# Kernel tuning notes

Measured on AMD Instinct MI355X. Metric: run time of the kernel, lower is better.

The kernel has to match this reference:

```python
import jax, jax.numpy as jnp
import numpy as np

N, E = 50000, 800000
IN, HID, HEADS, OUT, ED = 128, 64, 2, 64, 32
NEG_SLOPE = 0.2


def setup_inputs() -> dict:
    key = jax.random.key(0)
    ks = jax.random.split(key, 16)
    g = lambda i, shape: (jax.random.normal(ks[i], shape, jnp.float32) * 0.05)
    return {
        "x": g(0, (N, IN)),
        "edge_index": jax.random.randint(ks[1], (2, E), 0, N, jnp.int32),
        "edge_attr": g(2, (E, ED)),
        # layer 1 (heads=HEADS, out=HID)
        "Wl1": g(3, (IN, HEADS * HID)), "bl1": jnp.zeros((HEADS * HID,), jnp.float32),
        "Wr1": g(4, (IN, HEADS * HID)), "br1": jnp.zeros((HEADS * HID,), jnp.float32),
        "We1": g(5, (ED, HEADS * HID)),
        "att1": g(6, (HEADS, HID)),
        "bias1": jnp.zeros((HEADS * HID,), jnp.float32),
        # layer 2 (heads=1, out=OUT)
        "Wl2": g(7, (HEADS * HID, OUT)), "bl2": jnp.zeros((OUT,), jnp.float32),
        "Wr2": g(8, (HEADS * HID, OUT)), "br2": jnp.zeros((OUT,), jnp.float32),
        "We2": g(9, (ED, OUT)),
        "att2": g(10, (1, OUT)),
        "bias2": jnp.zeros((OUT,), jnp.float32),
    }


def _add_self_loops(src, dst, edge_attr, n):
    # PyG add_self_loops(fill_value='mean'): self-loop attr = mean of incoming edge attrs
    ones = jnp.ones((src.shape[0],), edge_attr.dtype)
    deg = jax.ops.segment_sum(ones, dst, num_segments=n)
    loop_attr = jax.ops.segment_sum(edge_attr, dst, num_segments=n) / jnp.maximum(deg, 1.0)[:, None]
    idx = jnp.arange(n, dtype=src.dtype)
    return (jnp.concatenate([src, idx]), jnp.concatenate([dst, idx]),
            jnp.concatenate([edge_attr, loop_attr], axis=0))


def _gatv2_layer(x, src, dst, edge_attr, Wl, bl, Wr, br, We, att, bias, heads, out_c):
    n = x.shape[0]
    xl = (x @ Wl + bl).reshape(n, heads, out_c)   # applied to source nodes j
    xr = (x @ Wr + br).reshape(n, heads, out_c)   # applied to target nodes i
    e = (edge_attr @ We).reshape(-1, heads, out_c)
    m = jax.nn.leaky_relu(xl[src] + xr[dst] + e, NEG_SLOPE)   # [E', H, C]
    logits = jnp.einsum('ehc,hc->eh', m, att)                  # [E', H]
    # segment softmax over incoming edges of each target node
    lmax = jax.ops.segment_max(logits, dst, num_segments=n)
    lmax = jnp.where(jnp.isfinite(lmax), lmax, 0.0)
    ex = jnp.exp(logits - lmax[dst])
    denom = jax.ops.segment_sum(ex, dst, num_segments=n)
    alpha = ex / (denom[dst] + 1e-16)                          # [E', H]
    out = jax.ops.segment_sum(xl[src] * alpha[:, :, None], dst, num_segments=n)
    return out.reshape(n, heads * out_c) + bias                # concat=True


def reference(x, edge_index, edge_attr,
              Wl1, bl1, Wr1, br1, We1, att1, bias1,
              Wl2, bl2, Wr2, br2, We2, att2, bias2):
    n = x.shape[0]
    src, dst, ea = _add_self_loops(edge_index[0], edge_index[1], edge_attr, n)
    h = _gatv2_layer(x, src, dst, ea, Wl1, bl1, Wr1, br1, We1, att1, bias1, HEADS, HID)
    h = jax.nn.elu(h)
    out = _gatv2_layer(h, src, dst, ea, Wl2, bl2, Wr2, br2, We2, att2, bias2, 1, OUT)
    return out
```

## Files before the change

kernel.cpp:

```cpp
#include <hip/hip_runtime.h>
#include <cmath>

#define NN 50000
#define EE 800000
#define H1C 128
#define OUTC 64
#define EDIM 32
#define NBLK 196

__device__ __forceinline__ float bcast(float v, int d) {
    return __int_as_float(__builtin_amdgcn_readlane(__float_as_int(v), d));
}


__global__ void k_hist(const int* __restrict__ ei, int* deg) {
    int e = blockIdx.x * 256 + threadIdx.x;
    if (e < EE) atomicAdd(&deg[ei[EE + e]], 1);
}

__global__ void k_scan_block(const int* __restrict__ deg, int* offs, int* bsum) {
    __shared__ int s[256];
    int t = threadIdx.x;
    int gid = blockIdx.x * 256 + t;
    int v = (gid < NN) ? deg[gid] : 0;
    s[t] = v;
    __syncthreads();
    for (int off = 1; off < 256; off <<= 1) {
        int add = (t >= off) ? s[t - off] : 0;
        __syncthreads();
        s[t] += add;
        __syncthreads();
    }
    if (gid < NN) offs[gid] = s[t] - v;
    if (t == 255) bsum[blockIdx.x] = s[255];
}

__global__ void k_scan_top(const int* __restrict__ bsum, int* bexcl) {
    __shared__ int s[256];
    int t = threadIdx.x;
    int v = (t < NBLK) ? bsum[t] : 0;
    s[t] = v;
    __syncthreads();
    for (int off = 1; off < 256; off <<= 1) {
        int add = (t >= off) ? s[t - off] : 0;
        __syncthreads();
        s[t] += add;
        __syncthreads();
    }
    bexcl[t] = s[t] - v;
}

__global__ void k_scan_add(int* offs, const int* __restrict__ bexcl) {
    int gid = blockIdx.x * 256 + threadIdx.x;
    if (gid < NN) offs[gid] += bexcl[blockIdx.x];
    if (gid == 0) offs[NN] = EE;
}

__global__ void k_scatter(const int* __restrict__ ei, const int* __restrict__ offs,
                          int* deg, int2* esort) {
    int e = blockIdx.x * 256 + threadIdx.x;
    if (e >= EE) return;
    int dst = ei[EE + e];
    int idx = atomicSub(&deg[dst], 1) - 1;
    esort[offs[dst] + idx] = make_int2(ei[e], e);
}


template <int MO, bool IL>
__global__ void k_lin_pair(const float* __restrict__ x,
                           const float* __restrict__ Wa, const float* __restrict__ ba,
                           const float* __restrict__ Wb, const float* __restrict__ bb,
                           float* __restrict__ oa, float* __restrict__ ob) {
    __shared__ float xsT[128][36];
    int n0 = blockIdx.x * 32;
    int nthr = 2 * MO;
    for (int idx = threadIdx.x; idx < 32 * 128; idx += nthr) {
        int n = idx >> 7, k = idx & 127;
        xsT[k][n] = (n0 + n < NN) ? x[(size_t)(n0 + n) * 128 + k] : 0.f;
    }
    __syncthreads();
    int t = threadIdx.x;
    const float* W  = (t < MO) ? Wa : Wb;
    const float* bp = (t < MO) ? ba : bb;
    float* op       = (t < MO) ? oa : ob;
    int m = (t < MO) ? t : t - MO;
    float bv = bp[m];
    float acc[32];
#pragma unroll
    for (int n = 0; n < 32; ++n) acc[n] = bv;
#pragma unroll 2
    for (int k = 0; k < 128; ++k) {
        float w = W[k * MO + m];
        const float4* row = reinterpret_cast<const float4*>(&xsT[k][0]);
#pragma unroll
        for (int c = 0; c < 8; ++c) {
            float4 v = row[c];
            acc[4 * c + 0] = fmaf(v.x, w, acc[4 * c + 0]);
            acc[4 * c + 1] = fmaf(v.y, w, acc[4 * c + 1]);
            acc[4 * c + 2] = fmaf(v.z, w, acc[4 * c + 2]);
            acc[4 * c + 3] = fmaf(v.w, w, acc[4 * c + 3]);
        }
    }
    int mo = IL ? (((m & 63) << 1) + (m >> 6)) : m;
#pragma unroll
    for (int n = 0; n < 32; ++n)
        if (n0 + n < NN) op[(size_t)(n0 + n) * MO + mo] = acc[n];
}


__device__ __forceinline__ void edge_upd1(float2 xlv, float av,
                                          float2 xrv, float a0, float a1,
                                          const float (&wr0)[32], const float (&wr1)[32],
                                          float& mr0, float& mr1, float& s0, float& s1,
                                          float& acc0, float& acc1) {
    float t0 = 0.f, t1 = 0.f, u0 = 0.f, u1 = 0.f;
#pragma unroll
    for (int d = 0; d < 16; ++d) {
        float a = bcast(av, d);
        t0 = fmaf(a, wr0[d], t0);
        t1 = fmaf(a, wr1[d], t1);
    }
#pragma unroll
    for (int d = 16; d < 32; ++d) {
        float a = bcast(av, d);
        u0 = fmaf(a, wr0[d], u0);
        u1 = fmaf(a, wr1[d], u1);
    }
    float m0 = (xlv.x + xrv.x) + (t0 + u0);
    float m1 = (xlv.y + xrv.y) + (t1 + u1);
    m0 = m0 > 0.f ? m0 : 0.2f * m0;
    m1 = m1 > 0.f ? m1 : 0.2f * m1;
    float p0 = m0 * a0, p1 = m1 * a1;
#pragma unroll
    for (int off = 32; off; off >>= 1) { p0 += __shfl_xor(p0, off); p1 += __shfl_xor(p1, off); }
    float nm = fmaxf(mr0, p0);
    float sc = __expf(mr0 - nm), e = __expf(p0 - nm);
    s0 = s0 * sc + e; acc0 = fmaf(acc0, sc, e * xlv.x); mr0 = nm;
    nm = fmaxf(mr1, p1);
    sc = __expf(mr1 - nm); e = __expf(p1 - nm);
    s1 = s1 * sc + e; acc1 = fmaf(acc1, sc, e * xlv.y); mr1 = nm;
}

__global__ void __launch_bounds__(256) k_l1(
    const int2* __restrict__ esort, const int* __restrict__ offs,
    const float* __restrict__ ea, const float* __restrict__ We,
    const float* __restrict__ att, const float* __restrict__ xl,
    const float* __restrict__ xr, const float* __restrict__ bias,
    float* __restrict__ hb) {
    int lane = threadIdx.x & 63;
    float wr0[32], wr1[32];
#pragma unroll
    for (int d = 0; d < 32; ++d) {
        wr0[d] = We[d * H1C + lane];
        wr1[d] = We[d * H1C + 64 + lane];
    }
    int dst = (blockIdx.x << 2) + (threadIdx.x >> 6);
    if (dst >= NN) return;
    int beg = offs[dst], end = offs[dst + 1];
    int n = end - beg;
    float a0 = att[lane], a1 = att[64 + lane];
    size_t db = (size_t)dst * H1C;
    float2 xrv = reinterpret_cast<const float2*>(xr + db)[lane];
    float mr0 = -INFINITY, mr1 = -INFINITY;
    float s0 = 0.f, s1 = 0.f, acc0 = 0.f, acc1 = 0.f, easum = 0.f;

    float2 xlv = make_float2(0.f, 0.f);
    float av = 0.f;
    if (n > 0) {
        int2 ed = esort[beg];
        xlv = reinterpret_cast<const float2*>(xl + (size_t)ed.x * H1C)[lane];
        av = ea[(size_t)ed.y * EDIM + (lane & 31)];
    }
    for (int j = beg; j < end; ++j) {
        float2 cxl = xlv; float cav = av;
        if (j + 1 < end) {
            int2 ed = esort[j + 1];
            xlv = reinterpret_cast<const float2*>(xl + (size_t)ed.x * H1C)[lane];
            av = ea[(size_t)ed.y * EDIM + (lane & 31)];
        }
        easum += cav;
        edge_upd1(cxl, cav, xrv, a0, a1, wr0, wr1, mr0, mr1, s0, s1, acc0, acc1);
    }

    float lav = easum * ((n > 0) ? (1.f / (float)n) : 1.f);
    float2 sxl = reinterpret_cast<const float2*>(xl + db)[lane];
    edge_upd1(sxl, lav, xrv, a0, a1, wr0, wr1, mr0, mr1, s0, s1, acc0, acc1);

    float h0 = acc0 / (s0 + 1e-16f) + bias[lane];
    float h1 = acc1 / (s1 + 1e-16f) + bias[64 + lane];
    hb[db + lane]      = h0 > 0.f ? h0 : expm1f(h0);
    hb[db + 64 + lane] = h1 > 0.f ? h1 : expm1f(h1);
}


__device__ __forceinline__ void edge_upd2(float xlv, float av, float xrv, float a,
                                          const float (&wr)[32],
                                          float& mr, float& s, float& acc) {
    float t = 0.f, u = 0.f;
#pragma unroll
    for (int d = 0; d < 16; ++d)
        t = fmaf(bcast(av, d), wr[d], t);
#pragma unroll
    for (int d = 16; d < 32; ++d)
        u = fmaf(bcast(av, d), wr[d], u);
    float m = (xlv + xrv) + (t + u);
    m = m > 0.f ? m : 0.2f * m;
    float p = m * a;
#pragma unroll
    for (int off = 32; off; off >>= 1) p += __shfl_xor(p, off);
    float nm = fmaxf(mr, p);
    float sc = __expf(mr - nm), e = __expf(p - nm);
    s = s * sc + e; acc = fmaf(acc, sc, e * xlv); mr = nm;
}

__global__ void __launch_bounds__(256) k_l2(
    const int2* __restrict__ esort, const int* __restrict__ offs,
    const float* __restrict__ ea, const float* __restrict__ We,
    const float* __restrict__ att, const float* __restrict__ xl,
    const float* __restrict__ xr, const float* __restrict__ bias,
    float* __restrict__ out) {
    int lane = threadIdx.x & 63;
    float wr[32];
#pragma unroll
    for (int d = 0; d < 32; ++d) wr[d] = We[d * OUTC + lane];
    int dst = (blockIdx.x << 2) + (threadIdx.x >> 6);
    if (dst >= NN) return;
    int beg = offs[dst], end = offs[dst + 1];
    int n = end - beg;
    float a = att[lane];
    size_t db = (size_t)dst * OUTC;
    float xrv = xr[db + lane];
    float mr = -INFINITY, s = 0.f, acc = 0.f, easum = 0.f;

    float xlv = 0.f, av = 0.f;
    if (n > 0) {
        int2 ed = esort[beg];
        xlv = xl[(size_t)ed.x * OUTC + lane];
        av = ea[(size_t)ed.y * EDIM + (lane & 31)];
    }
    for (int j = beg; j < end; ++j) {
        float cxl = xlv, cav = av;
        if (j + 1 < end) {
            int2 ed = esort[j + 1];
            xlv = xl[(size_t)ed.x * OUTC + lane];
            av = ea[(size_t)ed.y * EDIM + (lane & 31)];
        }
        easum += cav;
        edge_upd2(cxl, cav, xrv, a, wr, mr, s, acc);
    }
    float lav = easum * ((n > 0) ? (1.f / (float)n) : 1.f);
    float sxl = xl[db + lane];
    edge_upd2(sxl, lav, xrv, a, wr, mr, s, acc);

    out[db + lane] = acc / (s + 1e-16f) + bias[lane];
}


extern "C" void kernel_launch(void* const* d_in, const int* in_sizes, int n_in,
                              void* d_out, int out_size, void* d_ws, size_t ws_size,
                              hipStream_t stream) {
    const float* x    = (const float*)d_in[0];
    const int*   ei   = (const int*)d_in[1];
    const float* ea   = (const float*)d_in[2];
    const float* Wl1  = (const float*)d_in[3];
    const float* bl1  = (const float*)d_in[4];
    const float* Wr1  = (const float*)d_in[5];
    const float* br1  = (const float*)d_in[6];
    const float* We1  = (const float*)d_in[7];
    const float* att1 = (const float*)d_in[8];
    const float* bias1= (const float*)d_in[9];
    const float* Wl2  = (const float*)d_in[10];
    const float* bl2  = (const float*)d_in[11];
    const float* Wr2  = (const float*)d_in[12];
    const float* br2  = (const float*)d_in[13];
    const float* We2  = (const float*)d_in[14];
    const float* att2 = (const float*)d_in[15];
    const float* bias2= (const float*)d_in[16];
    float* out = (float*)d_out;

    char* w = (char*)d_ws;
    int2* esort = (int2*)w;                 w += (size_t)EE * 8;
    int*  offs  = (int*)w;                  w += (size_t)(NN + 4) * 4;
    int*  bsum  = (int*)w;                  w += 256 * 4;
    int*  bexcl = (int*)w;                  w += 256 * 4;
    int*  deg   = (int*)w;                  w += (size_t)NN * 4;
    float* xl1  = (float*)w;                w += (size_t)NN * H1C * 4;
    float* xr1  = (float*)w;                w += (size_t)NN * H1C * 4;
    float* hb   = (float*)w;                w += (size_t)NN * H1C * 4;
    float* xl2  = (float*)w;                w += (size_t)NN * OUTC * 4;
    float* xr2  = (float*)w;                w += (size_t)NN * OUTC * 4;

    hipMemsetAsync(deg, 0, (size_t)NN * 4, stream);

    k_hist<<<(EE + 255) / 256, 256, 0, stream>>>(ei, deg);
    k_scan_block<<<NBLK, 256, 0, stream>>>(deg, offs, bsum);
    k_scan_top<<<1, 256, 0, stream>>>(bsum, bexcl);
    k_scan_add<<<NBLK, 256, 0, stream>>>(offs, bexcl);
    k_scatter<<<(EE + 255) / 256, 256, 0, stream>>>(ei, offs, deg, esort);

    k_lin_pair<128, true><<<(NN + 31) / 32, 256, 0, stream>>>(x, Wl1, bl1, Wr1, br1, xl1, xr1);
    k_l1<<<(NN + 3) / 4, 256, 0, stream>>>(esort, offs, ea, We1, att1, xl1, xr1, bias1, hb);

    k_lin_pair<64, false><<<(NN + 31) / 32, 128, 0, stream>>>(hb, Wl2, bl2, Wr2, br2, xl2, xr2);
    k_l2<<<(NN + 3) / 4, 256, 0, stream>>>(esort, offs, ea, We2, att2, xl2, xr2, bias2, out);
}
```

Measured before the change: 857.0 us.

## Use DPP wave reductions and two-deep prefetch in edge-aggregation kernels

Replaces the shuffle-based 64-lane reduction of attention logits with a DPP row/broadcast reduction sequence that ends in a readlane. The per-edge loops in both GATv2 layers now keep two edges in flight, splitting the edge-attribute projection from the softmax update so loads for edge j+2/j+3 are issued while the current edge is processed. Launch bounds add a minimum-occupancy hint of 4. The deeper prefetch raises register pressure, and the occupancy hint may force spills given the 64 weight registers per lane.

```diff
diff --git a/kernel.cpp b/kernel.cpp
--- a/kernel.cpp
+++ b/kernel.cpp
@@ -10,6 +10,21 @@
 
 __device__ __forceinline__ float bcast(float v, int d) {
     return __int_as_float(__builtin_amdgcn_readlane(__float_as_int(v), d));
+}
+
+template <int CTRL, int RM>
+__device__ __forceinline__ float dpp_add(float x) {
+    int y = __builtin_amdgcn_update_dpp(0, __float_as_int(x), CTRL, RM, 0xf, false);
+    return x + __int_as_float(y);
+}
+__device__ __forceinline__ float wsum64(float x) {
+    x = dpp_add<0x111, 0xf>(x);
+    x = dpp_add<0x112, 0xf>(x);
+    x = dpp_add<0x114, 0xf>(x);
+    x = dpp_add<0x118, 0xf>(x);
+    x = dpp_add<0x142, 0xa>(x);
+    x = dpp_add<0x143, 0xc>(x);
+    return __int_as_float(__builtin_amdgcn_readlane(__float_as_int(x), 63));
 }
 
 
@@ -108,11 +123,8 @@
 }
 
 
-__device__ __forceinline__ void edge_upd1(float2 xlv, float av,
-                                          float2 xrv, float a0, float a1,
-                                          const float (&wr0)[32], const float (&wr1)[32],
-                                          float& mr0, float& mr1, float& s0, float& s1,
-                                          float& acc0, float& acc1) {
+__device__ __forceinline__ void dot1(float av, const float (&wr0)[32], const float (&wr1)[32],
+                                     float& q0, float& q1) {
     float t0 = 0.f, t1 = 0.f, u0 = 0.f, u1 = 0.f;
 #pragma unroll
     for (int d = 0; d < 16; ++d) {
@@ -126,13 +138,19 @@
         u0 = fmaf(a, wr0[d], u0);
         u1 = fmaf(a, wr1[d], u1);
     }
-    float m0 = (xlv.x + xrv.x) + (t0 + u0);
-    float m1 = (xlv.y + xrv.y) + (t1 + u1);
+    q0 = t0 + u0; q1 = t1 + u1;
+}
+
+__device__ __forceinline__ void fin1(float2 xlv, float q0, float q1, float2 xrv,
+                                     float a0, float a1,
+                                     float& mr0, float& mr1, float& s0, float& s1,
+                                     float& acc0, float& acc1) {
+    float m0 = (xlv.x + xrv.x) + q0;
+    float m1 = (xlv.y + xrv.y) + q1;
     m0 = m0 > 0.f ? m0 : 0.2f * m0;
     m1 = m1 > 0.f ? m1 : 0.2f * m1;
-    float p0 = m0 * a0, p1 = m1 * a1;
-#pragma unroll
-    for (int off = 32; off; off >>= 1) { p0 += __shfl_xor(p0, off); p1 += __shfl_xor(p1, off); }
+    float p0 = wsum64(m0 * a0);
+    float p1 = wsum64(m1 * a1);
     float nm = fmaxf(mr0, p0);
     float sc = __expf(mr0 - nm), e = __expf(p0 - nm);
     s0 = s0 * sc + e; acc0 = fmaf(acc0, sc, e * xlv.x); mr0 = nm;
@@ -141,7 +159,7 @@
     s1 = s1 * sc + e; acc1 = fmaf(acc1, sc, e * xlv.y); mr1 = nm;
 }
 
-__global__ void __launch_bounds__(256) k_l1(
+__global__ void __launch_bounds__(256, 4) k_l1(
     const int2* __restrict__ esort, const int* __restrict__ offs,
     const float* __restrict__ ea, const float* __restrict__ We,
     const float* __restrict__ att, const float* __restrict__ xl,
@@ -164,27 +182,52 @@
     float mr0 = -INFINITY, mr1 = -INFINITY;
     float s0 = 0.f, s1 = 0.f, acc0 = 0.f, acc1 = 0.f, easum = 0.f;
 
-    float2 xlv = make_float2(0.f, 0.f);
-    float av = 0.f;
+    float2 xlA = make_float2(0.f, 0.f), xlB = make_float2(0.f, 0.f);
+    float avA = 0.f, avB = 0.f;
     if (n > 0) {
         int2 ed = esort[beg];
-        xlv = reinterpret_cast<const float2*>(xl + (size_t)ed.x * H1C)[lane];
-        av = ea[(size_t)ed.y * EDIM + (lane & 31)];
-    }
-    for (int j = beg; j < end; ++j) {
-        float2 cxl = xlv; float cav = av;
-        if (j + 1 < end) {
-            int2 ed = esort[j + 1];
-            xlv = reinterpret_cast<const float2*>(xl + (size_t)ed.x * H1C)[lane];
-            av = ea[(size_t)ed.y * EDIM + (lane & 31)];
-        }
-        easum += cav;
-        edge_upd1(cxl, cav, xrv, a0, a1, wr0, wr1, mr0, mr1, s0, s1, acc0, acc1);
+        xlA = reinterpret_cast<const float2*>(xl + (size_t)ed.x * H1C)[lane];
+        avA = ea[(size_t)ed.y * EDIM + (lane & 31)];
+    }
+    if (n > 1) {
+        int2 ed = esort[beg + 1];
+        xlB = reinterpret_cast<const float2*>(xl + (size_t)ed.x * H1C)[lane];
+        avB = ea[(size_t)ed.y * EDIM + (lane & 31)];
+    }
+    int j = beg;
+    for (; j + 2 <= end; j += 2) {
+        float q0, q1;
+        easum += avA;
+        dot1(avA, wr0, wr1, q0, q1);
+        float2 c = xlA;
+        if (j + 2 < end) {
+            int2 ed = esort[j + 2];
+            xlA = reinterpret_cast<const float2*>(xl + (size_t)ed.x * H1C)[lane];
+            avA = ea[(size_t)ed.y * EDIM + (lane & 31)];
+        }
+        fin1(c, q0, q1, xrv, a0, a1, mr0, mr1, s0, s1, acc0, acc1);
+        easum += avB;
+        dot1(avB, wr0, wr1, q0, q1);
+        float2 d2 = xlB;
+        if (j + 3 < end) {
+            int2 ed = esort[j + 3];
+            xlB = reinterpret_cast<const float2*>(xl + (size_t)ed.x * H1C)[lane];
+            avB = ea[(size_t)ed.y * EDIM + (lane & 31)];
+        }
+        fin1(d2, q0, q1, xrv, a0, a1, mr0, mr1, s0, s1, acc0, acc1);
+    }
+    if (j < end) {
+        float q0, q1;
+        easum += avA;
+        dot1(avA, wr0, wr1, q0, q1);
+        fin1(xlA, q0, q1, xrv, a0, a1, mr0, mr1, s0, s1, acc0, acc1);
     }
 
     float lav = easum * ((n > 0) ? (1.f / (float)n) : 1.f);
+    float q0, q1;
+    dot1(lav, wr0, wr1, q0, q1);
     float2 sxl = reinterpret_cast<const float2*>(xl + db)[lane];
-    edge_upd1(sxl, lav, xrv, a0, a1, wr0, wr1, mr0, mr1, s0, s1, acc0, acc1);
+    fin1(sxl, q0, q1, xrv, a0, a1, mr0, mr1, s0, s1, acc0, acc1);
 
     float h0 = acc0 / (s0 + 1e-16f) + bias[lane];
     float h1 = acc1 / (s1 + 1e-16f) + bias[64 + lane];
@@ -193,27 +236,26 @@
 }
 
 
-__device__ __forceinline__ void edge_upd2(float xlv, float av, float xrv, float a,
-                                          const float (&wr)[32],
-                                          float& mr, float& s, float& acc) {
+__device__ __forceinline__ float dot2(float av, const float (&wr)[32]) {
     float t = 0.f, u = 0.f;
 #pragma unroll
-    for (int d = 0; d < 16; ++d)
-        t = fmaf(bcast(av, d), wr[d], t);
-#pragma unroll
-    for (int d = 16; d < 32; ++d)
-        u = fmaf(bcast(av, d), wr[d], u);
-    float m = (xlv + xrv) + (t + u);
+    for (int d = 0; d < 16; ++d) t = fmaf(bcast(av, d), wr[d], t);
+#pragma unroll
+    for (int d = 16; d < 32; ++d) u = fmaf(bcast(av, d), wr[d], u);
+    return t + u;
+}
+
+__device__ __forceinline__ void fin2(float xlv, float q, float xrv, float a,
+                                     float& mr, float& s, float& acc) {
+    float m = (xlv + xrv) + q;
     m = m > 0.f ? m : 0.2f * m;
-    float p = m * a;
-#pragma unroll
-    for (int off = 32; off; off >>= 1) p += __shfl_xor(p, off);
+    float p = wsum64(m * a);
     float nm = fmaxf(mr, p);
     float sc = __expf(mr - nm), e = __expf(p - nm);
     s = s * sc + e; acc = fmaf(acc, sc, e * xlv); mr = nm;
 }
 
-__global__ void __launch_bounds__(256) k_l2(
+__global__ void __launch_bounds__(256, 4) k_l2(
     const int2* __restrict__ esort, const int* __restrict__ offs,
     const float* __restrict__ ea, const float* __restrict__ We,
     const float* __restrict__ att, const float* __restrict__ xl,
@@ -232,25 +274,48 @@
     float xrv = xr[db + lane];
     float mr = -INFINITY, s = 0.f, acc = 0.f, easum = 0.f;
 
-    float xlv = 0.f, av = 0.f;
+    float xlA = 0.f, xlB = 0.f, avA = 0.f, avB = 0.f;
     if (n > 0) {
         int2 ed = esort[beg];
-        xlv = xl[(size_t)ed.x * OUTC + lane];
-        av = ea[(size_t)ed.y * EDIM + (lane & 31)];
-    }
-    for (int j = beg; j < end; ++j) {
-        float cxl = xlv, cav = av;
-        if (j + 1 < end) {
-            int2 ed = esort[j + 1];
-            xlv = xl[(size_t)ed.x * OUTC + lane];
-            av = ea[(size_t)ed.y * EDIM + (lane & 31)];
-        }
-        easum += cav;
-        edge_upd2(cxl, cav, xrv, a, wr, mr, s, acc);
-    }
+        xlA = xl[(size_t)ed.x * OUTC + lane];
+        avA = ea[(size_t)ed.y * EDIM + (lane & 31)];
+    }
+    if (n > 1) {
+        int2 ed = esort[beg + 1];
+        xlB = xl[(size_t)ed.x * OUTC + lane];
+        avB = ea[(size_t)ed.y * EDIM + (lane & 31)];
+    }
+    int j = beg;
+    for (; j + 2 <= end; j += 2) {
+        easum += avA;
+        float q = dot2(avA, wr);
+        float c = xlA;
+        if (j + 2 < end) {
+            int2 ed = esort[j + 2];
+            xlA = xl[(size_t)ed.x * OUTC + lane];
+            avA = ea[(size_t)ed.y * EDIM + (lane & 31)];
+        }
+        fin2(c, q, xrv, a, mr, s, acc);
+        easum += avB;
+        q = dot2(avB, wr);
+        float d2 = xlB;
+        if (j + 3 < end) {
+            int2 ed = esort[j + 3];
+            xlB = xl[(size_t)ed.x * OUTC + lane];
+            avB = ea[(size_t)ed.y * EDIM + (lane & 31)];
+        }
+        fin2(d2, q, xrv, a, mr, s, acc);
+    }
+    if (j < end) {
+        easum += avA;
+        float q = dot2(avA, wr);
+        fin2(xlA, q, xrv, a, mr, s, acc);
+    }
+
     float lav = easum * ((n > 0) ? (1.f / (float)n) : 1.f);
+    float q = dot2(lav, wr);
     float sxl = xl[db + lane];
-    edge_upd2(sxl, lav, xrv, a, wr, mr, s, acc);
+    fin2(sxl, q, xrv, a, mr, s, acc);
 
     out[db + lane] = acc / (s + 1e-16f) + bias[lane];
 }
@@ -290,7 +355,7 @@
     float* xl2  = (float*)w;                w += (size_t)NN * OUTC * 4;
     float* xr2  = (float*)w;                w += (size_t)NN * OUTC * 4;
 
-    hipMemsetAsync(deg, 0, (size_t)NN * 4, stream);
+    (void)hipMemsetAsync(deg, 0, (size_t)NN * 4, stream);
 
     k_hist<<<(EE + 255) / 256, 256, 0, stream>>>(ei, deg);
     k_scan_block<<<NBLK, 256, 0, stream>>>(deg, offs, bsum);
```

Result: faster. 809.7 us (-5.5%).

## Split layer-1 heads across wavefronts, DPP reductions, 4-deep edge prefetch

Applied to the files above, without the earlier changes.

Layer 1 now runs one wavefront per (destination, head) instead of one per destination handling both heads. This halves per-thread registers (one 32-float weight array) and raises occupancy via launch bounds. The projection writes xl/xr in a head-major planar layout so each head's gathers are contiguous 64-float rows. Edge processing in both layers uses a shared 4-deep software-pipelined gather loop, and the per-edge logit reduction switches from shuffle-xor to DPP row ops plus readlane. The trade-off is that edge indices and edge attributes are now gathered twice in layer 1, once per head.

```diff
diff --git a/kernel.cpp b/kernel.cpp
--- a/kernel.cpp
+++ b/kernel.cpp
@@ -10,6 +10,21 @@
 
 __device__ __forceinline__ float bcast(float v, int d) {
     return __int_as_float(__builtin_amdgcn_readlane(__float_as_int(v), d));
+}
+
+template <int CTRL, int RM>
+__device__ __forceinline__ float dpp_add(float x) {
+    int y = __builtin_amdgcn_update_dpp(0, __float_as_int(x), CTRL, RM, 0xf, false);
+    return x + __int_as_float(y);
+}
+__device__ __forceinline__ float wsum64(float x) {
+    x = dpp_add<0x111, 0xf>(x);
+    x = dpp_add<0x112, 0xf>(x);
+    x = dpp_add<0x114, 0xf>(x);
+    x = dpp_add<0x118, 0xf>(x);
+    x = dpp_add<0x142, 0xa>(x);
+    x = dpp_add<0x143, 0xc>(x);
+    return __int_as_float(__builtin_amdgcn_readlane(__float_as_int(x), 63));
 }
 
 
@@ -66,7 +81,7 @@
 }
 
 
-template <int MO, bool IL>
+template <int MO, int MODE>
 __global__ void k_lin_pair(const float* __restrict__ x,
                            const float* __restrict__ Wa, const float* __restrict__ ba,
                            const float* __restrict__ Wb, const float* __restrict__ bb,
@@ -101,119 +116,105 @@
             acc[4 * c + 3] = fmaf(v.w, w, acc[4 * c + 3]);
         }
     }
-    int mo = IL ? (((m & 63) << 1) + (m >> 6)) : m;
-#pragma unroll
-    for (int n = 0; n < 32; ++n)
-        if (n0 + n < NN) op[(size_t)(n0 + n) * MO + mo] = acc[n];
-}
-
-
-__device__ __forceinline__ void edge_upd1(float2 xlv, float av,
-                                          float2 xrv, float a0, float a1,
-                                          const float (&wr0)[32], const float (&wr1)[32],
-                                          float& mr0, float& mr1, float& s0, float& s1,
-                                          float& acc0, float& acc1) {
-    float t0 = 0.f, t1 = 0.f, u0 = 0.f, u1 = 0.f;
-#pragma unroll
-    for (int d = 0; d < 16; ++d) {
-        float a = bcast(av, d);
-        t0 = fmaf(a, wr0[d], t0);
-        t1 = fmaf(a, wr1[d], t1);
-    }
-#pragma unroll
-    for (int d = 16; d < 32; ++d) {
-        float a = bcast(av, d);
-        u0 = fmaf(a, wr0[d], u0);
-        u1 = fmaf(a, wr1[d], u1);
-    }
-    float m0 = (xlv.x + xrv.x) + (t0 + u0);
-    float m1 = (xlv.y + xrv.y) + (t1 + u1);
-    m0 = m0 > 0.f ? m0 : 0.2f * m0;
-    m1 = m1 > 0.f ? m1 : 0.2f * m1;
-    float p0 = m0 * a0, p1 = m1 * a1;
-#pragma unroll
-    for (int off = 32; off; off >>= 1) { p0 += __shfl_xor(p0, off); p1 += __shfl_xor(p1, off); }
-    float nm = fmaxf(mr0, p0);
-    float sc = __expf(mr0 - nm), e = __expf(p0 - nm);
-    s0 = s0 * sc + e; acc0 = fmaf(acc0, sc, e * xlv.x); mr0 = nm;
-    nm = fmaxf(mr1, p1);
-    sc = __expf(mr1 - nm); e = __expf(p1 - nm);
-    s1 = s1 * sc + e; acc1 = fmaf(acc1, sc, e * xlv.y); mr1 = nm;
-}
-
-__global__ void __launch_bounds__(256) k_l1(
+#pragma unroll
+    for (int n = 0; n < 32; ++n) {
+        if (n0 + n < NN) {
+            if (MODE == 2)
+                op[(size_t)(m >> 6) * NN * 64 + (size_t)(n0 + n) * 64 + (m & 63)] = acc[n];
+            else
+                op[(size_t)(n0 + n) * MO + m] = acc[n];
+        }
+    }
+}
+
+
+__device__ __forceinline__ float dotw(float av, const float (&wr)[32]) {
+    float t = 0.f, u = 0.f;
+#pragma unroll
+    for (int d = 0; d < 16; ++d) t = fmaf(bcast(av, d), wr[d], t);
+#pragma unroll
+    for (int d = 16; d < 32; ++d) u = fmaf(bcast(av, d), wr[d], u);
+    return t + u;
+}
+
+__device__ __forceinline__ void finw(float xlv, float q, float xrv, float a,
+                                     float& mr, float& s, float& acc) {
+    float m = (xlv + xrv) + q;
+    m = m > 0.f ? m : 0.2f * m;
+    float p = wsum64(m * a);
+    float nm = fmaxf(mr, p);
+    float sc = __expf(mr - nm), e = __expf(p - nm);
+    s = s * sc + e; acc = fmaf(acc, sc, e * xlv); mr = nm;
+}
+
+__device__ __forceinline__ void edge_scan(const int2* __restrict__ esort, int beg, int end,
+                                          const float* __restrict__ xlh,
+                                          const float* __restrict__ ea,
+                                          const float (&wr)[32], float xrv, float a, int lane,
+                                          float& mr, float& s, float& acc, float& easum) {
+    float xlA = 0.f, avA = 0.f, xlB = 0.f, avB = 0.f;
+    float xlC = 0.f, avC = 0.f, xlD = 0.f, avD = 0.f;
+#define RELOAD(S, J)                                                     \
+    if ((J) < end) {                                                     \
+        int2 ed = esort[(J)];                                            \
+        xl##S = xlh[(size_t)ed.x * 64 + lane];                           \
+        av##S = ea[(size_t)ed.y * EDIM + (lane & 31)];                   \
+    }
+#define PROC(S)                                                          \
+    do { easum += av##S; float q = dotw(av##S, wr);                      \
+         finw(xl##S, q, xrv, a, mr, s, acc); } while (0)
+    RELOAD(A, beg); RELOAD(B, beg + 1); RELOAD(C, beg + 2); RELOAD(D, beg + 3);
+    int j = beg;
+    for (; j + 4 <= end; j += 4) {
+        PROC(A); RELOAD(A, j + 4);
+        PROC(B); RELOAD(B, j + 5);
+        PROC(C); RELOAD(C, j + 6);
+        PROC(D); RELOAD(D, j + 7);
+    }
+    int rem = end - j;
+    if (rem > 0) PROC(A);
+    if (rem > 1) PROC(B);
+    if (rem > 2) PROC(C);
+#undef RELOAD
+#undef PROC
+}
+
+
+__global__ void __launch_bounds__(256, 8) k_l1(
     const int2* __restrict__ esort, const int* __restrict__ offs,
     const float* __restrict__ ea, const float* __restrict__ We,
     const float* __restrict__ att, const float* __restrict__ xl,
-    const float* __restrict__ xr, const float* __restrict__ bias,
-    float* __restrict__ hb) {
+    const float* __restrict__ xr,
+    const float* __restrict__ bias, float* __restrict__ hb) {
     int lane = threadIdx.x & 63;
-    float wr0[32], wr1[32];
-#pragma unroll
-    for (int d = 0; d < 32; ++d) {
-        wr0[d] = We[d * H1C + lane];
-        wr1[d] = We[d * H1C + 64 + lane];
-    }
-    int dst = (blockIdx.x << 2) + (threadIdx.x >> 6);
+    int w = threadIdx.x >> 6;
+    int head = w & 1;
+    int dst = blockIdx.x * 2 + (w >> 1);
     if (dst >= NN) return;
+    float wr[32];
+#pragma unroll
+    for (int d = 0; d < 32; ++d) wr[d] = We[d * H1C + head * 64 + lane];
+    const float* xlh = xl + (size_t)head * NN * 64;
+    const float* xrh = xr + (size_t)head * NN * 64;
     int beg = offs[dst], end = offs[dst + 1];
     int n = end - beg;
-    float a0 = att[lane], a1 = att[64 + lane];
-    size_t db = (size_t)dst * H1C;
-    float2 xrv = reinterpret_cast<const float2*>(xr + db)[lane];
-    float mr0 = -INFINITY, mr1 = -INFINITY;
-    float s0 = 0.f, s1 = 0.f, acc0 = 0.f, acc1 = 0.f, easum = 0.f;
-
-    float2 xlv = make_float2(0.f, 0.f);
-    float av = 0.f;
-    if (n > 0) {
-        int2 ed = esort[beg];
-        xlv = reinterpret_cast<const float2*>(xl + (size_t)ed.x * H1C)[lane];
-        av = ea[(size_t)ed.y * EDIM + (lane & 31)];
-    }
-    for (int j = beg; j < end; ++j) {
-        float2 cxl = xlv; float cav = av;
-        if (j + 1 < end) {
-            int2 ed = esort[j + 1];
-            xlv = reinterpret_cast<const float2*>(xl + (size_t)ed.x * H1C)[lane];
-            av = ea[(size_t)ed.y * EDIM + (lane & 31)];
-        }
-        easum += cav;
-        edge_upd1(cxl, cav, xrv, a0, a1, wr0, wr1, mr0, mr1, s0, s1, acc0, acc1);
-    }
+    float a = att[head * 64 + lane];
+    float xrv = xrh[(size_t)dst * 64 + lane];
+    float mr = -INFINITY, s = 0.f, acc = 0.f, easum = 0.f;
+
+    edge_scan(esort, beg, end, xlh, ea, wr, xrv, a, lane, mr, s, acc, easum);
 
     float lav = easum * ((n > 0) ? (1.f / (float)n) : 1.f);
-    float2 sxl = reinterpret_cast<const float2*>(xl + db)[lane];
-    edge_upd1(sxl, lav, xrv, a0, a1, wr0, wr1, mr0, mr1, s0, s1, acc0, acc1);
-
-    float h0 = acc0 / (s0 + 1e-16f) + bias[lane];
-    float h1 = acc1 / (s1 + 1e-16f) + bias[64 + lane];
-    hb[db + lane]      = h0 > 0.f ? h0 : expm1f(h0);
-    hb[db + 64 + lane] = h1 > 0.f ? h1 : expm1f(h1);
-}
-
-
-__device__ __forceinline__ void edge_upd2(float xlv, float av, float xrv, float a,
-                                          const float (&wr)[32],
-                                          float& mr, float& s, float& acc) {
-    float t = 0.f, u = 0.f;
-#pragma unroll
-    for (int d = 0; d < 16; ++d)
-        t = fmaf(bcast(av, d), wr[d], t);
-#pragma unroll
-    for (int d = 16; d < 32; ++d)
-        u = fmaf(bcast(av, d), wr[d], u);
-    float m = (xlv + xrv) + (t + u);
-    m = m > 0.f ? m : 0.2f * m;
-    float p = m * a;
-#pragma unroll
-    for (int off = 32; off; off >>= 1) p += __shfl_xor(p, off);
-    float nm = fmaxf(mr, p);
-    float sc = __expf(mr - nm), e = __expf(p - nm);
-    s = s * sc + e; acc = fmaf(acc, sc, e * xlv); mr = nm;
-}
-
-__global__ void __launch_bounds__(256) k_l2(
+    float q = dotw(lav, wr);
+    float sxl = xlh[(size_t)dst * 64 + lane];
+    finw(sxl, q, xrv, a, mr, s, acc);
+
+    float h = acc / (s + 1e-16f) + bias[head * 64 + lane];
+    hb[(size_t)dst * H1C + head * 64 + lane] = h > 0.f ? h : expm1f(h);
+}
+
+
+__global__ void __launch_bounds__(256, 8) k_l2(
     const int2* __restrict__ esort, const int* __restrict__ offs,
     const float* __restrict__ ea, const float* __restrict__ We,
     const float* __restrict__ att, const float* __restrict__ xl,
@@ -232,25 +233,12 @@
     float xrv = xr[db + lane];
     float mr = -INFINITY, s = 0.f, acc = 0.f, easum = 0.f;
 
-    float xlv = 0.f, av = 0.f;
-    if (n > 0) {
-        int2 ed = esort[beg];
-        xlv = xl[(size_t)ed.x * OUTC + lane];
-        av = ea[(size_t)ed.y * EDIM + (lane & 31)];
-    }
-    for (int j = beg; j < end; ++j) {
-        float cxl = xlv, cav = av;
-        if (j + 1 < end) {
-            int2 ed = esort[j + 1];
-            xlv = xl[(size_t)ed.x * OUTC + lane];
-            av = ea[(size_t)ed.y * EDIM + (lane & 31)];
-        }
-        easum += cav;
-        edge_upd2(cxl, cav, xrv, a, wr, mr, s, acc);
-    }
+    edge_scan(esort, beg, end, xl, ea, wr, xrv, a, lane, mr, s, acc, easum);
+
     float lav = easum * ((n > 0) ? (1.f / (float)n) : 1.f);
+    float q = dotw(lav, wr);
     float sxl = xl[db + lane];
-    edge_upd2(sxl, lav, xrv, a, wr, mr, s, acc);
+    finw(sxl, q, xrv, a, mr, s, acc);
 
     out[db + lane] = acc / (s + 1e-16f) + bias[lane];
 }
@@ -290,7 +278,7 @@
     float* xl2  = (float*)w;                w += (size_t)NN * OUTC * 4;
     float* xr2  = (float*)w;                w += (size_t)NN * OUTC * 4;
 
-    hipMemsetAsync(deg, 0, (size_t)NN * 4, stream);
+    (void)hipMemsetAsync(deg, 0, (size_t)NN * 4, stream);
 
     k_hist<<<(EE + 255) / 256, 256, 0, stream>>>(ei, deg);
     k_scan_block<<<NBLK, 256, 0, stream>>>(deg, offs, bsum);
@@ -298,9 +286,9 @@
     k_scan_add<<<NBLK, 256, 0, stream>>>(offs, bexcl);
     k_scatter<<<(EE + 255) / 256, 256, 0, stream>>>(ei, offs, deg, esort);
 
-    k_lin_pair<128, true><<<(NN + 31) / 32, 256, 0, stream>>>(x, Wl1, bl1, Wr1, br1, xl1, xr1);
-    k_l1<<<(NN + 3) / 4, 256, 0, stream>>>(esort, offs, ea, We1, att1, xl1, xr1, bias1, hb);
-
-    k_lin_pair<64, false><<<(NN + 31) / 32, 128, 0, stream>>>(hb, Wl2, bl2, Wr2, br2, xl2, xr2);
+    k_lin_pair<128, 2><<<(NN + 31) / 32, 256, 0, stream>>>(x, Wl1, bl1, Wr1, br1, xl1, xr1);
+    k_l1<<<(NN + 1) / 2, 256, 0, stream>>>(esort, offs, ea, We1, att1, xl1, xr1, bias1, hb);
+
+    k_lin_pair<64, 0><<<(NN + 31) / 32, 128, 0, stream>>>(hb, Wl2, bl2, Wr2, br2, xl2, xr2);
     k_l2<<<(NN + 3) / 4, 256, 0, stream>>>(esort, offs, ea, We2, att2, xl2, xr2, bias2, out);
 }
```

New measurement: 1.192 ms. +39.0%, slower.
